# Kernel optimization log

Hardware: AMD Instinct MI355X
Metric: run time of the kernel (lower is better)

Reference implementation:

```python
import jax, jax.numpy as jnp
import numpy as np

B, S, H, D = 32, 512, 768, 64  # batch, seq_len, hidden_size, inner_dim
BIG = 1e12


def _rope(x, sin_pos, cos_pos):
    # x: [B,S,D]; rotate pairs: [-x1, x0, -x3, x2, ...]
    x2 = jnp.stack([-x[..., 1::2], x[..., ::2]], axis=-1).reshape(x.shape)
    return x * cos_pos + x2 * sin_pos


def setup_inputs() -> dict:
    key = jax.random.key(0)
    k1, k2, k3 = jax.random.split(key, 3)
    hidden = jax.random.normal(k1, (B, S, H), dtype=jnp.float32)
    attention_mask = jnp.ones((B, S), dtype=jnp.float32)
    span_ids = jax.random.randint(k2, (B, S, S), 0, 2).astype(jnp.int32)
    dense_w = jax.random.normal(k3, (H, 2 * D), dtype=jnp.float32) * 0.02
    dense_b = jnp.zeros((2 * D,), dtype=jnp.float32)
    return {"hidden": hidden, "attention_mask": attention_mask,
            "span_ids": span_ids, "dense_w": dense_w, "dense_b": dense_b}


def reference(hidden, attention_mask, span_ids, dense_w, dense_b):
    b, s, _ = hidden.shape
    out = hidden @ dense_w + dense_b            # [B,S,2D]
    qw, kw = out[..., :D], out[..., D:]
    # sinusoidal position embedding, interleaved [s0,c0,s1,c1,...]
    pos = jnp.arange(s, dtype=jnp.float32)[:, None]              # [S,1]
    inv_freq = 10000.0 ** (-2.0 * jnp.arange(D // 2, dtype=jnp.float32) / D)
    ang = pos * inv_freq                                         # [S,D/2]
    sin_pos = jnp.repeat(jnp.sin(ang), 2, axis=-1)[None]         # [1,S,D]
    cos_pos = jnp.repeat(jnp.cos(ang), 2, axis=-1)[None]
    qw = _rope(qw, sin_pos, cos_pos)
    kw = _rope(kw, sin_pos, cos_pos)
    logits = jnp.einsum('bmd,bnd->bmn', qw, kw)                  # [B,S,S]
    pad = attention_mask[:, None, :]                             # mask keys (n)
    logits = logits * pad - (1.0 - pad) * BIG
    tril = jnp.tril(jnp.ones((s, s), logits.dtype), -1)          # strict lower
    logits = logits - tril * BIG
    logits = logits / (D ** 0.5)
    # multilabel categorical crossentropy over rows [B*S, S]
    y_true = span_ids.astype(logits.dtype).reshape(b * s, -1)
    y_pred = logits.reshape(b * s, -1)
    yp = (1.0 - 2.0 * y_true) * y_pred
    zeros = jnp.zeros((b * s, 1), yp.dtype)
    y_neg = jnp.concatenate([yp - y_true * BIG, zeros], axis=-1)
    y_pos = jnp.concatenate([yp - (1.0 - y_true) * BIG, zeros], axis=-1)
    loss = (jax.nn.logsumexp(y_neg, axis=-1) + jax.nn.logsumexp(y_pos, axis=-1)).mean()
    return loss
```

## Files before the change

kernel.cpp:

```cpp
#include <hip/hip_runtime.h>
#include <hip/hip_bf16.h>
#include <math.h>

#define Bb   32
#define Ss   512
#define Hh   768
#define Dd   64
#define ND   128
#define Mrows (Bb*Ss)
#define BIGF  1.0e12f
#define BIG8F 1.25e11f
#define NEGHUGE -1.0e30f

typedef __attribute__((ext_vector_type(8))) short short8;
typedef __attribute__((ext_vector_type(4))) float floatx4;

__device__ __forceinline__ short f2bf(float x) {
    unsigned u = __builtin_bit_cast(unsigned, x);
    u = (u + 0x7FFF + ((u >> 16) & 1)) >> 16;
    return (short)u;
}

__global__ __launch_bounds__(256) void prep_kernel(
    const float* __restrict__ w, short* __restrict__ wfrag,
    float2* __restrict__ rt, double* __restrict__ partial,
    unsigned* __restrict__ cnt)
{
    int idx = blockIdx.x * 256 + threadIdx.x;
    int j    = idx & 7;
    int lane = (idx >> 3) & 63;
    int rest = idx >> 9;
    int c    = rest % 24;
    int tt   = rest / 24;
    int n    = tt * 16 + (lane & 15);
    int k    = c * 32 + (lane >> 4) * 8 + j;
    wfrag[idx] = f2bf(w[k * ND + n]);
    if (idx < Ss * 32) {
        int spos = idx >> 5;
        int i    = idx & 31;
        float ln_base = -logf(10000.0f) / 32.0f;
        float invf = expf(ln_base * (float)i);
        float sn, cs;
        sincosf((float)spos * invf, &sn, &cs);
        rt[idx] = make_float2(sn, cs);
    }
    if (idx < 512) partial[idx] = 0.0;
    if (idx == 512) *cnt = 0u;
}

__global__ __launch_bounds__(512, 4) void proj_rope_kernel(
    const float*  __restrict__ hidden,
    const short*  __restrict__ wfrag,
    const float*  __restrict__ bias,
    const float2* __restrict__ rt,
    short* __restrict__ qbf,
    short* __restrict__ kbf)
{
    const int tid   = threadIdx.x;
    const int w     = tid >> 6;
    const int lane  = tid & 63;
    const int quad  = lane >> 4;
    const int l15   = lane & 15;
    const int rg    = w & 1;
    const int h     = (w >> 1) & 1;
    const int kh    = w >> 2;
    const int mrow0 = blockIdx.x * 32 + rg * 16;

    const float* ap  = hidden + (size_t)(mrow0 + l15) * Hh + quad * 8
                              + kh * 12 * 32;
    const short* bp0 = wfrag + (size_t)(h * 4) * 24 * 512 + lane * 8
                             + kh * 12 * 512;

    floatx4 acc[4] = {{0.f,0.f,0.f,0.f},{0.f,0.f,0.f,0.f},
                      {0.f,0.f,0.f,0.f},{0.f,0.f,0.f,0.f}};

    float4 A0[2], A1[2];
    short8 Bf[2][4];

#define PLOAD(buf, c) do {                                        \
    A0[buf] = *(const float4*)(ap + (c) * 32);                    \
    A1[buf] = *(const float4*)(ap + (c) * 32 + 4);                \
    Bf[buf][0] = *(const short8*)(bp0 + 0 * 24 * 512 + (c) * 512);\
    Bf[buf][1] = *(const short8*)(bp0 + 1 * 24 * 512 + (c) * 512);\
    Bf[buf][2] = *(const short8*)(bp0 + 2 * 24 * 512 + (c) * 512);\
    Bf[buf][3] = *(const short8*)(bp0 + 3 * 24 * 512 + (c) * 512);\
} while (0)

#define PCOMP(buf) do {                                         \
    short8 av;                                                  \
    av[0] = f2bf(A0[buf].x); av[1] = f2bf(A0[buf].y);           \
    av[2] = f2bf(A0[buf].z); av[3] = f2bf(A0[buf].w);           \
    av[4] = f2bf(A1[buf].x); av[5] = f2bf(A1[buf].y);           \
    av[6] = f2bf(A1[buf].z); av[7] = f2bf(A1[buf].w);           \
    acc[0] = __builtin_amdgcn_mfma_f32_16x16x32_bf16(av, Bf[buf][0], acc[0], 0, 0, 0); \
    acc[1] = __builtin_amdgcn_mfma_f32_16x16x32_bf16(av, Bf[buf][1], acc[1], 0, 0, 0); \
    acc[2] = __builtin_amdgcn_mfma_f32_16x16x32_bf16(av, Bf[buf][2], acc[2], 0, 0, 0); \
    acc[3] = __builtin_amdgcn_mfma_f32_16x16x32_bf16(av, Bf[buf][3], acc[3], 0, 0, 0); \
} while (0)

    PLOAD(0, 0);
    #pragma unroll
    for (int cc = 0; cc < 6; ++cc) {
        if (2 * cc + 1 < 12) PLOAD(1, 2 * cc + 1);
        PCOMP(0);
        if (2 * cc + 2 < 12) PLOAD(0, 2 * cc + 2);
        PCOMP(1);
    }
#undef PLOAD
#undef PCOMP

    __shared__ float lacc[4][16][64];
    const int slot = w & 3;
    if (kh == 1) {
        #pragma unroll
        for (int t = 0; t < 4; ++t)
            #pragma unroll
            for (int reg = 0; reg < 4; ++reg)
                lacc[slot][t * 4 + reg][lane] = acc[t][reg];
    }
    __syncthreads();
    if (kh == 1) return;

    #pragma unroll
    for (int t = 0; t < 4; ++t)
        #pragma unroll
        for (int reg = 0; reg < 4; ++reg)
            acc[t][reg] += lacc[slot][t * 4 + reg][lane];

    short* dst = h ? kbf : qbf;
    const float* bptr = bias + h * 64;
    const float qs = h ? 1.0f : 0.125f;

    #pragma unroll
    for (int t = 0; t < 4; ++t) {
        const int d  = t * 16 + l15;
        const float bz = bptr[d];
        const float2* rtp = rt + (d >> 1);
        #pragma unroll
        for (int reg = 0; reg < 4; ++reg) {
            const int grow = mrow0 + quad * 4 + reg;
            const int spos = grow & (Ss - 1);
            float2 sc = rtp[spos * 32];
            float x  = acc[t][reg] + bz;
            float xo = __shfl_xor(x, 1);
            float o  = (d & 1) ? (x * sc.y + xo * sc.x)
                               : (x * sc.y - xo * sc.x);
            dst[(size_t)grow * Dd + d] = f2bf(o * qs);
        }
    }
}

__global__ __launch_bounds__(512, 4) void span_loss_kernel(
    const short* __restrict__ qbf,
    const short* __restrict__ kbf,
    const float* __restrict__ mask,
    const int*   __restrict__ span,
    double* __restrict__ partial,
    unsigned* __restrict__ cnt,
    float* __restrict__ out)
{
    const int b    = blockIdx.x >> 4;
    const int m0   = (blockIdx.x & 15) * 32;
    const int tid  = threadIdx.x;
    const int w    = tid >> 6;
    const int lane = tid & 63;
    const int quad = lane >> 4;
    const int l15  = lane & 15;
    const int rh   = w & 1;
    const int cg   = w >> 1;
    const int rbase = m0 + rh * 16;
    const int cbase = cg * 128;

    __shared__ float part[2][4][32];
    __shared__ float bred[2][32];
    __shared__ int   isLast;

    int spv[8][4];
    float pdv[8];
    {
        const int* spp = span + ((size_t)(b * Ss + rbase + quad * 4)) * Ss
                              + cbase + l15;
        #pragma unroll
        for (int t = 0; t < 8; ++t) {
            pdv[t] = mask[b * Ss + cbase + t * 16 + l15];
            #pragma unroll
            for (int reg = 0; reg < 4; ++reg)
                spv[t][reg] = spp[(size_t)reg * Ss + t * 16];
        }
    }

    const short* qp = qbf + (size_t)(b * Ss + rbase + l15) * Dd + quad * 8;
    short8 a0 = *(const short8*)(qp);
    short8 a1 = *(const short8*)(qp + 32);

    floatx4 acc[8];
    #pragma unroll
    for (int t = 0; t < 8; ++t) acc[t] = (floatx4){0.f, 0.f, 0.f, 0.f};

    const short* kp = kbf + (size_t)(b * Ss + cbase + l15) * Dd + quad * 8;
    #pragma unroll
    for (int t = 0; t < 8; ++t) {
        short8 bv = *(const short8*)(kp + (size_t)t * 16 * Dd);
        acc[t] = __builtin_amdgcn_mfma_f32_16x16x32_bf16(a0, bv, acc[t], 0, 0, 0);
    }
    #pragma unroll
    for (int t = 0; t < 8; ++t) {
        short8 bv = *(const short8*)(kp + (size_t)t * 16 * Dd + 32);
        acc[t] = __builtin_amdgcn_mfma_f32_16x16x32_bf16(a1, bv, acc[t], 0, 0, 0);
    }

    unsigned spb = 0;
    #pragma unroll
    for (int t = 0; t < 8; ++t) {
        const int n = cbase + t * 16 + l15;
        const float pd = pdv[t];
        #pragma unroll
        for (int reg = 0; reg < 4; ++reg) {
            const int m = rbase + quad * 4 + reg;
            const int sv = spv[t][reg];
            float logit = acc[t][reg] * pd - (1.0f - pd) * BIG8F;
            if (n < m) logit -= BIG8F;
            acc[t][reg] = sv ? -logit : logit;
            spb |= (unsigned)(sv != 0) << (t * 4 + reg);
        }
    }

    float mxn[4] = {0.f, 0.f, 0.f, 0.f};
    float mxp[4] = {0.f, 0.f, 0.f, 0.f};
    #pragma unroll
    for (int t = 0; t < 8; ++t) {
        #pragma unroll
        for (int reg = 0; reg < 4; ++reg) {
            bool f = (spb >> (t * 4 + reg)) & 1u;
            float yp = acc[t][reg];
            mxn[reg] = fmaxf(mxn[reg], f ? NEGHUGE : yp);
            mxp[reg] = fmaxf(mxp[reg], f ? yp : NEGHUGE);
        }
    }
    #pragma unroll
    for (int off = 1; off < 16; off <<= 1) {
        #pragma unroll
        for (int reg = 0; reg < 4; ++reg) {
            mxn[reg] = fmaxf(mxn[reg], __shfl_xor(mxn[reg], off));
            mxp[reg] = fmaxf(mxp[reg], __shfl_xor(mxp[reg], off));
        }
    }
    if (l15 == 0) {
        #pragma unroll
        for (int reg = 0; reg < 4; ++reg) {
            part[0][cg][rh * 16 + quad * 4 + reg] = mxn[reg];
            part[1][cg][rh * 16 + quad * 4 + reg] = mxp[reg];
        }
    }
    __syncthreads();
    if (tid < 64) {
        int np = tid >> 5, r = tid & 31;
        float mv = fmaxf(fmaxf(part[np][0][r], part[np][1][r]),
                         fmaxf(part[np][2][r], part[np][3][r]));
        bred[np][r] = mv;
    }
    __syncthreads();

    float bmn[4], bmp[4];
    #pragma unroll
    for (int reg = 0; reg < 4; ++reg) {
        bmn[reg] = bred[0][rh * 16 + quad * 4 + reg];
        bmp[reg] = bred[1][rh * 16 + quad * 4 + reg];
    }
    float smn[4] = {0.f, 0.f, 0.f, 0.f};
    float smp[4] = {0.f, 0.f, 0.f, 0.f};
    #pragma unroll
    for (int t = 0; t < 8; ++t) {
        #pragma unroll
        for (int reg = 0; reg < 4; ++reg) {
            bool f = (spb >> (t * 4 + reg)) & 1u;
            float yp = acc[t][reg];
            smn[reg] += __expf((f ? NEGHUGE : yp) - bmn[reg]);
            smp[reg] += __expf((f ? yp : NEGHUGE) - bmp[reg]);
        }
    }
    #pragma unroll
    for (int off = 1; off < 16; off <<= 1) {
        #pragma unroll
        for (int reg = 0; reg < 4; ++reg) {
            smn[reg] += __shfl_xor(smn[reg], off);
            smp[reg] += __shfl_xor(smp[reg], off);
        }
    }
    if (l15 == 0) {
        #pragma unroll
        for (int reg = 0; reg < 4; ++reg) {
            part[0][cg][rh * 16 + quad * 4 + reg] = smn[reg];
            part[1][cg][rh * 16 + quad * 4 + reg] = smp[reg];
        }
    }
    __syncthreads();

    float lse = 0.0f;
    if (tid < 32) {
        int r = tid;
        float SN = __expf(-bred[0][r])
                 + part[0][0][r] + part[0][1][r] + part[0][2][r] + part[0][3][r];
        float SP = __expf(-bred[1][r])
                 + part[1][0][r] + part[1][1][r] + part[1][2][r] + part[1][3][r];
        lse = (bred[0][r] + logf(SN)) + (bred[1][r] + logf(SP));
    }
    if (tid < 64) {
        double dv = (tid < 32) ? (double)lse : 0.0;
        #pragma unroll
        for (int off = 1; off < 32; off <<= 1) dv += __shfl_xor(dv, off);
        if (tid == 0) {
            partial[blockIdx.x] = dv;
            __threadfence();
            unsigned old = atomicAdd(cnt, 1u);
            isLast = (old == 511u) ? 1 : 0;
        }
    }
    __syncthreads();

    if (isLast && tid < 64) {
        double s = 0.0;
        #pragma unroll
        for (int i = 0; i < 8; ++i)
            s += atomicAdd(&partial[tid + i * 64], 0.0);
        #pragma unroll
        for (int off = 1; off < 64; off <<= 1) s += __shfl_xor(s, off);
        if (tid == 0) out[0] = (float)(s / (double)Mrows);
    }
}

extern "C" void kernel_launch(void* const* d_in, const int* in_sizes, int n_in,
                              void* d_out, int out_size, void* d_ws, size_t ws_size,
                              hipStream_t stream)
{
    const float* hidden = (const float*)d_in[0];
    const float* mask   = (const float*)d_in[1];
    const int*   span   = (const int*)  d_in[2];
    const float* w      = (const float*)d_in[3];
    const float* bias   = (const float*)d_in[4];
    float* out = (float*)d_out;

    char* p = (char*)d_ws;
    double*   partial = (double*)p;
    unsigned* cnt     = (unsigned*)(p + 4096);
    short*    wfrag   = (short*)(p + 8192);
    float2*   rt      = (float2*)(p + 8192 + 196608);
    short*    qbf     = (short*)(p + 8192 + 196608 + 131072);
    short*    kbf     = qbf + (size_t)Mrows * Dd;

    prep_kernel<<<Hh * ND / 256, 256, 0, stream>>>(w, wfrag, rt, partial, cnt);
    proj_rope_kernel<<<Mrows / 32, 512, 0, stream>>>(hidden, wfrag, bias, rt, qbf, kbf);
    span_loss_kernel<<<Bb * 16, 512, 0, stream>>>(qbf, kbf, mask, span, partial, cnt, out);
}
```

Measured before the change: 153.0 us.

## Split span-loss blocks to 16 rows, use atomic double sum, single exp

The span loss kernel now runs 1024 blocks of 256 threads, each covering 16 query rows, where it used to run 512 blocks of 512 threads covering 32 rows. This is meant to give more blocks for load balancing across CUs. The final reduction drops the per-block partial array and the last-block gather in favour of a single double atomicAdd per block. The LSE accumulation now computes one exp per element instead of two by picking the row max according to the label. The trade-off is more contention on one global atomic and a smaller block granularity.

```diff
diff --git a/kernel.cpp b/kernel.cpp
--- a/kernel.cpp
+++ b/kernel.cpp
@@ -23,7 +23,7 @@
 
 __global__ __launch_bounds__(256) void prep_kernel(
     const float* __restrict__ w, short* __restrict__ wfrag,
-    float2* __restrict__ rt, double* __restrict__ partial,
+    float2* __restrict__ rt, double* __restrict__ dsum,
     unsigned* __restrict__ cnt)
 {
     int idx = blockIdx.x * 256 + threadIdx.x;
@@ -44,8 +44,8 @@
         sincosf((float)spos * invf, &sn, &cs);
         rt[idx] = make_float2(sn, cs);
     }
-    if (idx < 512) partial[idx] = 0.0;
-    if (idx == 512) *cnt = 0u;
+    if (idx == 0) *dsum = 0.0;
+    if (idx == 1) *cnt = 0u;
 }
 
 __global__ __launch_bounds__(512, 4) void proj_rope_kernel(
@@ -150,35 +150,32 @@
     }
 }
 
-__global__ __launch_bounds__(512, 4) void span_loss_kernel(
+__global__ __launch_bounds__(256, 4) void span_loss_kernel(
     const short* __restrict__ qbf,
     const short* __restrict__ kbf,
     const float* __restrict__ mask,
     const int*   __restrict__ span,
-    double* __restrict__ partial,
+    double* __restrict__ dsum,
     unsigned* __restrict__ cnt,
     float* __restrict__ out)
 {
-    const int b    = blockIdx.x >> 4;
-    const int m0   = (blockIdx.x & 15) * 32;
+    const int b    = blockIdx.x >> 5;
+    const int m0   = (blockIdx.x & 31) * 16;
     const int tid  = threadIdx.x;
     const int w    = tid >> 6;
     const int lane = tid & 63;
     const int quad = lane >> 4;
     const int l15  = lane & 15;
-    const int rh   = w & 1;
-    const int cg   = w >> 1;
-    const int rbase = m0 + rh * 16;
-    const int cbase = cg * 128;
-
-    __shared__ float part[2][4][32];
-    __shared__ float bred[2][32];
+    const int cbase = w * 128;
+
+    __shared__ float part[2][4][16];
+    __shared__ float bred[2][16];
     __shared__ int   isLast;
 
     int spv[8][4];
     float pdv[8];
     {
-        const int* spp = span + ((size_t)(b * Ss + rbase + quad * 4)) * Ss
+        const int* spp = span + ((size_t)(b * Ss + m0 + quad * 4)) * Ss
                               + cbase + l15;
         #pragma unroll
         for (int t = 0; t < 8; ++t) {
@@ -189,7 +186,7 @@
         }
     }
 
-    const short* qp = qbf + (size_t)(b * Ss + rbase + l15) * Dd + quad * 8;
+    const short* qp = qbf + (size_t)(b * Ss + m0 + l15) * Dd + quad * 8;
     short8 a0 = *(const short8*)(qp);
     short8 a1 = *(const short8*)(qp + 32);
 
@@ -216,7 +213,7 @@
         const float pd = pdv[t];
         #pragma unroll
         for (int reg = 0; reg < 4; ++reg) {
-            const int m = rbase + quad * 4 + reg;
+            const int m = m0 + quad * 4 + reg;
             const int sv = spv[t][reg];
             float logit = acc[t][reg] * pd - (1.0f - pd) * BIG8F;
             if (n < m) logit -= BIG8F;
@@ -248,13 +245,13 @@
     if (l15 == 0) {
         #pragma unroll
         for (int reg = 0; reg < 4; ++reg) {
-            part[0][cg][rh * 16 + quad * 4 + reg] = mxn[reg];
-            part[1][cg][rh * 16 + quad * 4 + reg] = mxp[reg];
-        }
-    }
-    __syncthreads();
-    if (tid < 64) {
-        int np = tid >> 5, r = tid & 31;
+            part[0][w][quad * 4 + reg] = mxn[reg];
+            part[1][w][quad * 4 + reg] = mxp[reg];
+        }
+    }
+    __syncthreads();
+    if (tid < 32) {
+        int np = tid >> 4, r = tid & 15;
         float mv = fmaxf(fmaxf(part[np][0][r], part[np][1][r]),
                          fmaxf(part[np][2][r], part[np][3][r]));
         bred[np][r] = mv;
@@ -264,8 +261,8 @@
     float bmn[4], bmp[4];
     #pragma unroll
     for (int reg = 0; reg < 4; ++reg) {
-        bmn[reg] = bred[0][rh * 16 + quad * 4 + reg];
-        bmp[reg] = bred[1][rh * 16 + quad * 4 + reg];
+        bmn[reg] = bred[0][quad * 4 + reg];
+        bmp[reg] = bred[1][quad * 4 + reg];
     }
     float smn[4] = {0.f, 0.f, 0.f, 0.f};
     float smp[4] = {0.f, 0.f, 0.f, 0.f};
@@ -275,8 +272,9 @@
         for (int reg = 0; reg < 4; ++reg) {
             bool f = (spb >> (t * 4 + reg)) & 1u;
             float yp = acc[t][reg];
-            smn[reg] += __expf((f ? NEGHUGE : yp) - bmn[reg]);
-            smp[reg] += __expf((f ? yp : NEGHUGE) - bmp[reg]);
+            float e = __expf(yp - (f ? bmp[reg] : bmn[reg]));
+            smn[reg] += f ? 0.0f : e;
+            smp[reg] += f ? e : 0.0f;
         }
     }
     #pragma unroll
@@ -290,14 +288,14 @@
     if (l15 == 0) {
         #pragma unroll
         for (int reg = 0; reg < 4; ++reg) {
-            part[0][cg][rh * 16 + quad * 4 + reg] = smn[reg];
-            part[1][cg][rh * 16 + quad * 4 + reg] = smp[reg];
+            part[0][w][quad * 4 + reg] = smn[reg];
+            part[1][w][quad * 4 + reg] = smp[reg];
         }
     }
     __syncthreads();
 
     float lse = 0.0f;
-    if (tid < 32) {
+    if (tid < 16) {
         int r = tid;
         float SN = __expf(-bred[0][r])
                  + part[0][0][r] + part[0][1][r] + part[0][2][r] + part[0][3][r];
@@ -306,26 +304,21 @@
         lse = (bred[0][r] + logf(SN)) + (bred[1][r] + logf(SP));
     }
     if (tid < 64) {
-        double dv = (tid < 32) ? (double)lse : 0.0;
-        #pragma unroll
-        for (int off = 1; off < 32; off <<= 1) dv += __shfl_xor(dv, off);
+        double dv = (tid < 16) ? (double)lse : 0.0;
+        #pragma unroll
+        for (int off = 1; off < 16; off <<= 1) dv += __shfl_xor(dv, off);
         if (tid == 0) {
-            partial[blockIdx.x] = dv;
+            atomicAdd(dsum, dv);
             __threadfence();
             unsigned old = atomicAdd(cnt, 1u);
-            isLast = (old == 511u) ? 1 : 0;
-        }
-    }
-    __syncthreads();
-
-    if (isLast && tid < 64) {
-        double s = 0.0;
-        #pragma unroll
-        for (int i = 0; i < 8; ++i)
-            s += atomicAdd(&partial[tid + i * 64], 0.0);
-        #pragma unroll
-        for (int off = 1; off < 64; off <<= 1) s += __shfl_xor(s, off);
-        if (tid == 0) out[0] = (float)(s / (double)Mrows);
+            isLast = (old == (unsigned)(Bb * 32 - 1)) ? 1 : 0;
+        }
+    }
+    __syncthreads();
+
+    if (isLast && tid == 0) {
+        double s = atomicAdd(dsum, 0.0);
+        out[0] = (float)(s / (double)Mrows);
     }
 }
 
@@ -341,14 +334,14 @@
     float* out = (float*)d_out;
 
     char* p = (char*)d_ws;
-    double*   partial = (double*)p;
-    unsigned* cnt     = (unsigned*)(p + 4096);
-    short*    wfrag   = (short*)(p + 8192);
-    float2*   rt      = (float2*)(p + 8192 + 196608);
-    short*    qbf     = (short*)(p + 8192 + 196608 + 131072);
-    short*    kbf     = qbf + (size_t)Mrows * Dd;
-
-    prep_kernel<<<Hh * ND / 256, 256, 0, stream>>>(w, wfrag, rt, partial, cnt);
+    double*   dsum = (double*)p;
+    unsigned* cnt  = (unsigned*)(p + 8);
+    short*    wfrag = (short*)(p + 8192);
+    float2*   rt    = (float2*)(p + 8192 + 196608);
+    short*    qbf   = (short*)(p + 8192 + 196608 + 131072);
+    short*    kbf   = qbf + (size_t)Mrows * Dd;
+
+    prep_kernel<<<Hh * ND / 256, 256, 0, stream>>>(w, wfrag, rt, dsum, cnt);
     proj_rope_kernel<<<Mrows / 32, 512, 0, stream>>>(hidden, wfrag, bias, rt, qbf, kbf);
-    span_loss_kernel<<<Bb * 16, 512, 0, stream>>>(qbf, kbf, mask, span, partial, cnt, out);
-}
+    span_loss_kernel<<<Bb * 32, 256, 0, stream>>>(qbf, kbf, mask, span, dsum, cnt, out);
+}
```

Result: slower. 170.0 us (+11.1%).
